# Kernel optimization log

Hardware: AMD Instinct MI355X
Metric: run time of the kernel (lower is better)

Reference implementation:

```python
import jax, jax.numpy as jnp
import numpy as np

B, T, F = 4096, 512, 8
U1, U2, DH = 8, 16, 16  # GRU1 units, GRU2 units, dense hidden


def _gru(x, W, Uw, b, units):
    """Keras GRU (v2, reset_after=True), activation=relu, recurrent_activation=sigmoid.
    x: [B, T, F_in]; W: [F_in, 3u]; Uw: [u, 3u]; b: [2, 3u]. Returns [B, T, u]."""
    bi, br = b[0], b[1]
    # precompute input projections for all timesteps: [T, B, 3u] (time-major for scan)
    gx = jnp.einsum('btf,fg->tbg', x, W) + bi
    u = units

    def step(h, xt):
        inner = h @ Uw + br                      # [B, 3u]
        z = jax.nn.sigmoid(xt[:, :u] + inner[:, :u])
        r = jax.nn.sigmoid(xt[:, u:2 * u] + inner[:, u:2 * u])
        hh = jax.nn.relu(xt[:, 2 * u:] + r * inner[:, 2 * u:])
        h = z * h + (1.0 - z) * hh
        return h, h

    h0 = jnp.zeros((x.shape[0], u), dtype=x.dtype)
    _, ys = jax.lax.scan(step, h0, gx)           # ys: [T, B, u]
    return jnp.transpose(ys, (1, 0, 2))          # [B, T, u]


def setup_inputs() -> dict:
    key = jax.random.key(0)
    ks = jax.random.split(key, 12)
    s = lambda fan_in: 1.0 / np.sqrt(fan_in)
    x = jax.random.normal(ks[0], (B, T, F), dtype=jnp.float32)
    W1 = jax.random.normal(ks[1], (F, 3 * U1), dtype=jnp.float32) * s(F)
    Ur1 = jax.random.normal(ks[2], (U1, 3 * U1), dtype=jnp.float32) * s(U1)
    b1 = jnp.zeros((2, 3 * U1), dtype=jnp.float32)
    W2 = jax.random.normal(ks[3], (U1, 3 * U2), dtype=jnp.float32) * s(U1)
    Ur2 = jax.random.normal(ks[4], (U2, 3 * U2), dtype=jnp.float32) * s(U2)
    b2 = jnp.zeros((2, 3 * U2), dtype=jnp.float32)
    Wd = jax.random.normal(ks[5], (U2, DH), dtype=jnp.float32) * 0.05  # random_normal init
    bd = jnp.zeros((DH,), dtype=jnp.float32)
    Wo = jax.random.normal(ks[6], (DH, 1), dtype=jnp.float32) * s(DH)
    bo = jnp.zeros((1,), dtype=jnp.float32)
    return {"x": x, "W1": W1, "Ur1": Ur1, "b1": b1, "W2": W2, "Ur2": Ur2,
            "b2": b2, "Wd": Wd, "bd": bd, "Wo": Wo, "bo": bo}


def reference(x, W1, Ur1, b1, W2, Ur2, b2, Wd, bd, Wo, bo):
    # Dropout layers are identity at inference (training=False)
    h = _gru(x, W1, Ur1, b1, U1)                 # [B, T, 8]
    h = _gru(h, W2, Ur2, b2, U2)                 # [B, T, 16]
    h = jax.nn.relu(h @ Wd + bd)                 # [B, T, 16]
    out = h @ Wo + bo                            # [B, T, 1]
    return out
```

## Files before the change

### kernel.cpp

```cpp
#include <hip/hip_runtime.h>

#define TT 512
#define LOG2E 1.44269504088896340736f

typedef float f2 __attribute__((ext_vector_type(2)));

template <int N>
__device__ __forceinline__ int rorki_(int v) {
    return __builtin_amdgcn_update_dpp(v, v, 0x120 + N, 0xf, 0xf, true);
}
template <int N>
__device__ __forceinline__ float rorkf_(float v) { return __int_as_float(rorki_<N>(__float_as_int(v))); }
template <int C>
__device__ __forceinline__ float shrf_(float v) {
    return __int_as_float(__builtin_amdgcn_update_dpp(0, __float_as_int(v), C, 0xf, 0xf, true));
}
__device__ __forceinline__ float sgm_(float v) {
    return __builtin_amdgcn_rcpf(1.f + __builtin_amdgcn_exp2f(-v));
}
__device__ __forceinline__ f2 pfma_(f2 a, f2 b, f2 c) {
    return __builtin_elementwise_fma(a, b, c);
}

__launch_bounds__(64)
__attribute__((amdgpu_waves_per_eu(1, 1)))
__global__ void gru_pk4(const float* __restrict__ x,
                        const float* __restrict__ W1, const float* __restrict__ Ur1,
                        const float* __restrict__ b1,
                        const float* __restrict__ W2, const float* __restrict__ Ur2,
                        const float* __restrict__ b2,
                        const float* __restrict__ Wd, const float* __restrict__ bd,
                        const float* __restrict__ Wo, const float* __restrict__ bo,
                        float* __restrict__ out)
{
    const int lane = threadIdx.x & 63;
    const int g    = lane >> 4;
    const int j    = lane & 15;
    const int u1   = j & 7;
    const int hi   = j >> 3;
    const int gcol = u1 + 8 * hi;
    const int row  = blockIdx.x * 4 + g;
    const bool ishi = (hi != 0);
    const bool isw  = (j == 15);

    const float* xbase = x + (size_t)blockIdx.x * 4 * TT * 8;
    const int    xoff  = g * TT * 8 + u1;
    float* outrow = out + (size_t)row * TT;

    int Lk[16];
    Lk[0]  = j;
    Lk[1]  = rorki_<1>(j);   Lk[2]  = rorki_<2>(j);   Lk[3]  = rorki_<3>(j);
    Lk[4]  = rorki_<4>(j);   Lk[5]  = rorki_<5>(j);   Lk[6]  = rorki_<6>(j);
    Lk[7]  = rorki_<7>(j);   Lk[8]  = rorki_<8>(j);   Lk[9]  = rorki_<9>(j);
    Lk[10] = rorki_<10>(j);  Lk[11] = rorki_<11>(j);  Lk[12] = rorki_<12>(j);
    Lk[13] = rorki_<13>(j);  Lk[14] = rorki_<14>(j);  Lk[15] = rorki_<15>(j);

    f2 Pz[8], Pr[8], Ph[8], Pd[8];
#pragma unroll
    for (int k = 0; k < 8; ++k) {
        const int a = Lk[2 * k], b = Lk[2 * k + 1];
        Pz[k] = f2{LOG2E * Ur2[a * 48 + j],      LOG2E * Ur2[b * 48 + j]};
        Pr[k] = f2{LOG2E * Ur2[a * 48 + 16 + j], LOG2E * Ur2[b * 48 + 16 + j]};
        Ph[k] = f2{Ur2[a * 48 + 32 + j],         Ur2[b * 48 + 32 + j]};
        Pd[k] = f2{Wd[a * 16 + j],               Wd[b * 16 + j]};
    }
    f2 Vz[4], Vr[4], Vh[4], VC[4], VQ[4];
    f2 Gx[4], Hx[4];
#pragma unroll
    for (int k = 0; k < 4; ++k) {
        const int a = Lk[2 * k] & 7, b = Lk[2 * k + 1] & 7;
        Vz[k] = f2{LOG2E * W2[a * 48 + j],       LOG2E * W2[b * 48 + j]};
        Vr[k] = f2{LOG2E * W2[a * 48 + 16 + j],  LOG2E * W2[b * 48 + 16 + j]};
        Vh[k] = f2{W2[a * 48 + 32 + j],          W2[b * 48 + 32 + j]};
        VC[k] = f2{LOG2E * Ur1[a * 24 + gcol],   LOG2E * Ur1[b * 24 + gcol]};
        VQ[k] = f2{Ur1[a * 24 + 16 + u1],        Ur1[b * 24 + 16 + u1]};
        Gx[k] = f2{LOG2E * W1[a * 24 + gcol],    LOG2E * W1[b * 24 + gcol]};
        Hx[k] = f2{W1[a * 24 + 16 + u1],         W1[b * 24 + 16 + u1]};
    }
    const float bAzr = LOG2E * (b1[gcol] + b1[24 + gcol]);
    const float bGh  = b1[16 + u1];
    const float bIh  = b1[40 + u1];
    const float bA2  = LOG2E * (b2[j] + b2[48 + j]);
    const float bB2  = LOG2E * (b2[16 + j] + b2[64 + j]);
    const float bC2  = b2[80 + j];
    const float bD2  = b2[32 + j];
    const float bdj  = bd[j], woj = Wo[j], boo = bo[0];

    float h1own = 0.f, h2own = 0.f;
    float azrP = bAzr, ihP = bIh;

    float xA = xbase[0 * 8 + xoff];
    float xB = xbase[1 * 8 + xoff];
    float xC = xbase[2 * 8 + xoff];

#define GSTEP(SS, XCUR, XFILL)                                                   \
    {                                                                            \
        const int s = (SS);                                                      \
                       \
        const float h0 = h2own;                                                  \
        f2 tp[8];                                                                \
        tp[0] = f2{h0,             rorkf_<1>(h0)};                               \
        tp[1] = f2{rorkf_<2>(h0),  rorkf_<3>(h0)};                               \
        tp[2] = f2{rorkf_<4>(h0),  rorkf_<5>(h0)};                               \
        tp[3] = f2{rorkf_<6>(h0),  rorkf_<7>(h0)};                               \
        tp[4] = f2{rorkf_<8>(h0),  rorkf_<9>(h0)};                               \
        tp[5] = f2{rorkf_<10>(h0), rorkf_<11>(h0)};                              \
        tp[6] = f2{rorkf_<12>(h0), rorkf_<13>(h0)};                              \
        tp[7] = f2{rorkf_<14>(h0), rorkf_<15>(h0)};                              \
        f2 za = f2{bA2, 0.f}, ra = f2{bB2, 0.f};                                 \
        f2 ha = f2{bC2, 0.f}, da = f2{bdj, 0.f};                                 \
        _Pragma("unroll")                                                        \
        for (int k = 0; k < 8; ++k) {                                            \
            za = pfma_(tp[k], Pz[k], za);  ra = pfma_(tp[k], Pr[k], ra);         \
            ha = pfma_(tp[k], Ph[k], ha);  da = pfma_(tp[k], Pd[k], da);         \
        }                                                                        \
                                     \
        const float x0 = XCUR;                                                   \
        f2 xp[4];                                                                \
        xp[0] = f2{x0,            rorkf_<1>(x0)};                                \
        xp[1] = f2{rorkf_<2>(x0), rorkf_<3>(x0)};                                \
        xp[2] = f2{rorkf_<4>(x0), rorkf_<5>(x0)};                                \
        xp[3] = f2{rorkf_<6>(x0), rorkf_<7>(x0)};                                \
        f2 axp = f2{azrP, 0.f}, ghp = f2{bGh, 0.f};                              \
        _Pragma("unroll")                                                        \
        for (int k = 0; k < 4; ++k) {                                            \
            axp = pfma_(xp[k], Gx[k], axp);  ghp = pfma_(xp[k], Hx[k], ghp);     \
        }                                                                        \
        XFILL = xbase[((s + 3) & (TT - 1)) * 8 + xoff];        \
                \
        const float azrC = axp.x + axp.y;                                        \
        const float s_own = sgm_(azrC);                                          \
        const float s_sw  = rorkf_<8>(s_own);                                    \
        const float z1 = ishi ? s_sw : s_own;                                    \
        const float r1 = ishi ? s_own : s_sw;                                    \
        const float ghxC = ghp.x + ghp.y;                                        \
        const float hh1 = fmaxf(fmaf(r1, ihP, ghxC), 0.f);                       \
        h1own = fmaf(z1, h1own - hh1, hh1);                                      \
                   \
        const float n0 = h1own;                                                  \
        f2 np[4];                                                                \
        np[0] = f2{n0,            rorkf_<1>(n0)};                                \
        np[1] = f2{rorkf_<2>(n0), rorkf_<3>(n0)};                                \
        np[2] = f2{rorkf_<4>(n0), rorkf_<5>(n0)};                                \
        np[3] = f2{rorkf_<6>(n0), rorkf_<7>(n0)};                                \
        f2 hbp = f2{bD2, 0.f}, aNp = f2{bAzr, 0.f}, iNp = f2{bIh, 0.f};          \
        _Pragma("unroll")                                                        \
        for (int k = 0; k < 4; ++k) {                                            \
            za  = pfma_(np[k], Vz[k], za);   ra  = pfma_(np[k], Vr[k], ra);      \
            hbp = pfma_(np[k], Vh[k], hbp);                                      \
            aNp = pfma_(np[k], VC[k], aNp);  iNp = pfma_(np[k], VQ[k], iNp);     \
        }                                                                        \
        azrP = aNp.x + aNp.y;  ihP = iNp.x + iNp.y;                              \
                                                  \
        const float zaC = za.x + za.y, raC = ra.x + ra.y;                        \
        const float haC = ha.x + ha.y, hbC = hbp.x + hbp.y;                      \
        const float z2 = sgm_(zaC), r2 = sgm_(raC);                              \
        const float hh2 = fmaxf(fmaf(r2, haC, hbC), 0.f);                        \
        h2own = fmaf(z2, h2own - hh2, hh2);                                      \
                                       \
        float e = fmaxf(da.x + da.y, 0.f) * woj;                                 \
        e += shrf_<0x118>(e);                                                    \
        e += shrf_<0x114>(e);                                                    \
        e += shrf_<0x112>(e);                                                    \
        e += shrf_<0x111>(e);                                                    \
        if (s > 0) { if (isw) outrow[s - 1] = e + boo; }                         \
    }

    for (int s0 = 0; s0 < TT; s0 += 4) {
        GSTEP(s0 + 0, xA, xA)
        GSTEP(s0 + 1, xB, xB)
        GSTEP(s0 + 2, xC, xC)
        GSTEP(s0 + 3, xA, xA)
        { float t = xB; xB = xC; xC = xA; xA = t; }
    }
#undef GSTEP

    {
        const float h0 = h2own;
        f2 tp[8];
        tp[0] = f2{h0,             rorkf_<1>(h0)};
        tp[1] = f2{rorkf_<2>(h0),  rorkf_<3>(h0)};
        tp[2] = f2{rorkf_<4>(h0),  rorkf_<5>(h0)};
        tp[3] = f2{rorkf_<6>(h0),  rorkf_<7>(h0)};
        tp[4] = f2{rorkf_<8>(h0),  rorkf_<9>(h0)};
        tp[5] = f2{rorkf_<10>(h0), rorkf_<11>(h0)};
        tp[6] = f2{rorkf_<12>(h0), rorkf_<13>(h0)};
        tp[7] = f2{rorkf_<14>(h0), rorkf_<15>(h0)};
        f2 da = f2{bdj, 0.f};
#pragma unroll
        for (int k = 0; k < 8; ++k) da = pfma_(tp[k], Pd[k], da);
        float e = fmaxf(da.x + da.y, 0.f) * woj;
        e += shrf_<0x118>(e);
        e += shrf_<0x114>(e);
        e += shrf_<0x112>(e);
        e += shrf_<0x111>(e);
        if (isw) outrow[TT - 1] = e + boo;
    }
}

extern "C" void kernel_launch(void* const* d_in, const int* in_sizes, int n_in,
                              void* d_out, int out_size, void* d_ws, size_t ws_size,
                              hipStream_t stream) {
    const float* x   = (const float*)d_in[0];
    const float* W1  = (const float*)d_in[1];
    const float* Ur1 = (const float*)d_in[2];
    const float* b1  = (const float*)d_in[3];
    const float* W2  = (const float*)d_in[4];
    const float* Ur2 = (const float*)d_in[5];
    const float* b2  = (const float*)d_in[6];
    const float* Wd  = (const float*)d_in[7];
    const float* bd  = (const float*)d_in[8];
    const float* Wo  = (const float*)d_in[9];
    const float* bo  = (const float*)d_in[10];
    float* out = (float*)d_out;

    dim3 grid(4096 / 4);
    dim3 block(64);
    gru_pk4<<<grid, block, 0, stream>>>(x, W1, Ur1, b1, W2, Ur2, b2,
                                        Wd, bd, Wo, bo, out);
}
```

Baseline: 174.6 us.

## Split GRU layers across two wavefronts with chunked LDS pipeline

```diff
diff --git a/kernel.cpp b/kernel.cpp
--- a/kernel.cpp
+++ b/kernel.cpp
@@ -1,6 +1,9 @@
 #include <hip/hip_runtime.h>
 
 #define TT 512
+#define CH 32
+#define NCH 16
+#define NPH (NCH + 2)
 #define LOG2E 1.44269504088896340736f
 
 typedef float f2 __attribute__((ext_vector_type(2)));
@@ -22,30 +25,30 @@
     return __builtin_elementwise_fma(a, b, c);
 }
 
-__launch_bounds__(64)
-__attribute__((amdgpu_waves_per_eu(1, 1)))
-__global__ void gru_pk4(const float* __restrict__ x,
-                        const float* __restrict__ W1, const float* __restrict__ Ur1,
-                        const float* __restrict__ b1,
-                        const float* __restrict__ W2, const float* __restrict__ Ur2,
-                        const float* __restrict__ b2,
-                        const float* __restrict__ Wd, const float* __restrict__ bd,
-                        const float* __restrict__ Wo, const float* __restrict__ bo,
-                        float* __restrict__ out)
+__launch_bounds__(128)
+__attribute__((amdgpu_waves_per_eu(2, 2)))
+__global__ void gru_ws(const float* __restrict__ x,
+                       const float* __restrict__ W1, const float* __restrict__ Ur1,
+                       const float* __restrict__ b1,
+                       const float* __restrict__ W2, const float* __restrict__ Ur2,
+                       const float* __restrict__ b2,
+                       const float* __restrict__ Wd, const float* __restrict__ bd,
+                       const float* __restrict__ Wo, const float* __restrict__ bo,
+                       float* __restrict__ out)
 {
-    const int lane = threadIdx.x & 63;
+    __shared__ float h1b[2][CH][4][8];
+    __shared__ float h2b[2][CH][4][16];
+
+    const int tid  = threadIdx.x;
+    const int wv   = tid >> 6;
+    const int lane = tid & 63;
     const int g    = lane >> 4;
     const int j    = lane & 15;
     const int u1   = j & 7;
     const int hi   = j >> 3;
     const int gcol = u1 + 8 * hi;
-    const int row  = blockIdx.x * 4 + g;
     const bool ishi = (hi != 0);
     const bool isw  = (j == 15);
-
-    const float* xbase = x + (size_t)blockIdx.x * 4 * TT * 8;
-    const int    xoff  = g * TT * 8 + u1;
-    float* outrow = out + (size_t)row * TT;
 
     int Lk[16];
     Lk[0]  = j;
@@ -55,146 +58,208 @@
     Lk[10] = rorki_<10>(j);  Lk[11] = rorki_<11>(j);  Lk[12] = rorki_<12>(j);
     Lk[13] = rorki_<13>(j);  Lk[14] = rorki_<14>(j);  Lk[15] = rorki_<15>(j);
 
-    f2 Pz[8], Pr[8], Ph[8], Pd[8];
-#pragma unroll
-    for (int k = 0; k < 8; ++k) {
-        const int a = Lk[2 * k], b = Lk[2 * k + 1];
-        Pz[k] = f2{LOG2E * Ur2[a * 48 + j],      LOG2E * Ur2[b * 48 + j]};
-        Pr[k] = f2{LOG2E * Ur2[a * 48 + 16 + j], LOG2E * Ur2[b * 48 + 16 + j]};
-        Ph[k] = f2{Ur2[a * 48 + 32 + j],         Ur2[b * 48 + 32 + j]};
-        Pd[k] = f2{Wd[a * 16 + j],               Wd[b * 16 + j]};
-    }
-    f2 Vz[4], Vr[4], Vh[4], VC[4], VQ[4];
-    f2 Gx[4], Hx[4];
-#pragma unroll
-    for (int k = 0; k < 4; ++k) {
-        const int a = Lk[2 * k] & 7, b = Lk[2 * k + 1] & 7;
-        Vz[k] = f2{LOG2E * W2[a * 48 + j],       LOG2E * W2[b * 48 + j]};
-        Vr[k] = f2{LOG2E * W2[a * 48 + 16 + j],  LOG2E * W2[b * 48 + 16 + j]};
-        Vh[k] = f2{W2[a * 48 + 32 + j],          W2[b * 48 + 32 + j]};
-        VC[k] = f2{LOG2E * Ur1[a * 24 + gcol],   LOG2E * Ur1[b * 24 + gcol]};
-        VQ[k] = f2{Ur1[a * 24 + 16 + u1],        Ur1[b * 24 + 16 + u1]};
-        Gx[k] = f2{LOG2E * W1[a * 24 + gcol],    LOG2E * W1[b * 24 + gcol]};
-        Hx[k] = f2{W1[a * 24 + 16 + u1],         W1[b * 24 + 16 + u1]};
-    }
-    const float bAzr = LOG2E * (b1[gcol] + b1[24 + gcol]);
-    const float bGh  = b1[16 + u1];
-    const float bIh  = b1[40 + u1];
-    const float bA2  = LOG2E * (b2[j] + b2[48 + j]);
-    const float bB2  = LOG2E * (b2[16 + j] + b2[64 + j]);
-    const float bC2  = b2[80 + j];
-    const float bD2  = b2[32 + j];
-    const float bdj  = bd[j], woj = Wo[j], boo = bo[0];
-
-    float h1own = 0.f, h2own = 0.f;
-    float azrP = bAzr, ihP = bIh;
-
-    float xA = xbase[0 * 8 + xoff];
-    float xB = xbase[1 * 8 + xoff];
-    float xC = xbase[2 * 8 + xoff];
-
-#define GSTEP(SS, XCUR, XFILL)                                                   \
-    {                                                                            \
-        const int s = (SS);                                                      \
-                       \
-        const float h0 = h2own;                                                  \
-        f2 tp[8];                                                                \
-        tp[0] = f2{h0,             rorkf_<1>(h0)};                               \
-        tp[1] = f2{rorkf_<2>(h0),  rorkf_<3>(h0)};                               \
-        tp[2] = f2{rorkf_<4>(h0),  rorkf_<5>(h0)};                               \
-        tp[3] = f2{rorkf_<6>(h0),  rorkf_<7>(h0)};                               \
-        tp[4] = f2{rorkf_<8>(h0),  rorkf_<9>(h0)};                               \
-        tp[5] = f2{rorkf_<10>(h0), rorkf_<11>(h0)};                              \
-        tp[6] = f2{rorkf_<12>(h0), rorkf_<13>(h0)};                              \
-        tp[7] = f2{rorkf_<14>(h0), rorkf_<15>(h0)};                              \
-        f2 za = f2{bA2, 0.f}, ra = f2{bB2, 0.f};                                 \
-        f2 ha = f2{bC2, 0.f}, da = f2{bdj, 0.f};                                 \
-        _Pragma("unroll")                                                        \
-        for (int k = 0; k < 8; ++k) {                                            \
-            za = pfma_(tp[k], Pz[k], za);  ra = pfma_(tp[k], Pr[k], ra);         \
-            ha = pfma_(tp[k], Ph[k], ha);  da = pfma_(tp[k], Pd[k], da);         \
-        }                                                                        \
-                                     \
-        const float x0 = XCUR;                                                   \
-        f2 xp[4];                                                                \
-        xp[0] = f2{x0,            rorkf_<1>(x0)};                                \
-        xp[1] = f2{rorkf_<2>(x0), rorkf_<3>(x0)};                                \
-        xp[2] = f2{rorkf_<4>(x0), rorkf_<5>(x0)};                                \
-        xp[3] = f2{rorkf_<6>(x0), rorkf_<7>(x0)};                                \
-        f2 axp = f2{azrP, 0.f}, ghp = f2{bGh, 0.f};                              \
-        _Pragma("unroll")                                                        \
-        for (int k = 0; k < 4; ++k) {                                            \
-            axp = pfma_(xp[k], Gx[k], axp);  ghp = pfma_(xp[k], Hx[k], ghp);     \
-        }                                                                        \
-        XFILL = xbase[((s + 3) & (TT - 1)) * 8 + xoff];        \
-                \
-        const float azrC = axp.x + axp.y;                                        \
-        const float s_own = sgm_(azrC);                                          \
-        const float s_sw  = rorkf_<8>(s_own);                                    \
-        const float z1 = ishi ? s_sw : s_own;                                    \
-        const float r1 = ishi ? s_own : s_sw;                                    \
-        const float ghxC = ghp.x + ghp.y;                                        \
-        const float hh1 = fmaxf(fmaf(r1, ihP, ghxC), 0.f);                       \
-        h1own = fmaf(z1, h1own - hh1, hh1);                                      \
-                   \
-        const float n0 = h1own;                                                  \
-        f2 np[4];                                                                \
-        np[0] = f2{n0,            rorkf_<1>(n0)};                                \
-        np[1] = f2{rorkf_<2>(n0), rorkf_<3>(n0)};                                \
-        np[2] = f2{rorkf_<4>(n0), rorkf_<5>(n0)};                                \
-        np[3] = f2{rorkf_<6>(n0), rorkf_<7>(n0)};                                \
-        f2 hbp = f2{bD2, 0.f}, aNp = f2{bAzr, 0.f}, iNp = f2{bIh, 0.f};          \
-        _Pragma("unroll")                                                        \
-        for (int k = 0; k < 4; ++k) {                                            \
-            za  = pfma_(np[k], Vz[k], za);   ra  = pfma_(np[k], Vr[k], ra);      \
-            hbp = pfma_(np[k], Vh[k], hbp);                                      \
-            aNp = pfma_(np[k], VC[k], aNp);  iNp = pfma_(np[k], VQ[k], iNp);     \
-        }                                                                        \
-        azrP = aNp.x + aNp.y;  ihP = iNp.x + iNp.y;                              \
-                                                  \
-        const float zaC = za.x + za.y, raC = ra.x + ra.y;                        \
-        const float haC = ha.x + ha.y, hbC = hbp.x + hbp.y;                      \
-        const float z2 = sgm_(zaC), r2 = sgm_(raC);                              \
-        const float hh2 = fmaxf(fmaf(r2, haC, hbC), 0.f);                        \
-        h2own = fmaf(z2, h2own - hh2, hh2);                                      \
-                                       \
-        float e = fmaxf(da.x + da.y, 0.f) * woj;                                 \
-        e += shrf_<0x118>(e);                                                    \
-        e += shrf_<0x114>(e);                                                    \
-        e += shrf_<0x112>(e);                                                    \
-        e += shrf_<0x111>(e);                                                    \
-        if (s > 0) { if (isw) outrow[s - 1] = e + boo; }                         \
-    }
-
-    for (int s0 = 0; s0 < TT; s0 += 4) {
-        GSTEP(s0 + 0, xA, xA)
-        GSTEP(s0 + 1, xB, xB)
-        GSTEP(s0 + 2, xC, xC)
-        GSTEP(s0 + 3, xA, xA)
-        { float t = xB; xB = xC; xC = xA; xA = t; }
-    }
-#undef GSTEP
-
-    {
-        const float h0 = h2own;
-        f2 tp[8];
-        tp[0] = f2{h0,             rorkf_<1>(h0)};
-        tp[1] = f2{rorkf_<2>(h0),  rorkf_<3>(h0)};
-        tp[2] = f2{rorkf_<4>(h0),  rorkf_<5>(h0)};
-        tp[3] = f2{rorkf_<6>(h0),  rorkf_<7>(h0)};
-        tp[4] = f2{rorkf_<8>(h0),  rorkf_<9>(h0)};
-        tp[5] = f2{rorkf_<10>(h0), rorkf_<11>(h0)};
-        tp[6] = f2{rorkf_<12>(h0), rorkf_<13>(h0)};
-        tp[7] = f2{rorkf_<14>(h0), rorkf_<15>(h0)};
-        f2 da = f2{bdj, 0.f};
-#pragma unroll
-        for (int k = 0; k < 8; ++k) da = pfma_(tp[k], Pd[k], da);
-        float e = fmaxf(da.x + da.y, 0.f) * woj;
-        e += shrf_<0x118>(e);
-        e += shrf_<0x114>(e);
-        e += shrf_<0x112>(e);
-        e += shrf_<0x111>(e);
-        if (isw) outrow[TT - 1] = e + boo;
+    if (wv == 0) {
+        f2 Gx[4], Hx[4], VC[4], VQ[4];
+#pragma unroll
+        for (int k = 0; k < 4; ++k) {
+            const int a = Lk[2 * k] & 7, b = Lk[2 * k + 1] & 7;
+            Gx[k] = f2{LOG2E * W1[a * 24 + gcol],  LOG2E * W1[b * 24 + gcol]};
+            Hx[k] = f2{W1[a * 24 + 16 + u1],       W1[b * 24 + 16 + u1]};
+            VC[k] = f2{LOG2E * Ur1[a * 24 + gcol], LOG2E * Ur1[b * 24 + gcol]};
+            VQ[k] = f2{Ur1[a * 24 + 16 + u1],      Ur1[b * 24 + 16 + u1]};
+        }
+        f2 Pd[8];
+#pragma unroll
+        for (int k = 0; k < 8; ++k)
+            Pd[k] = f2{Wd[(2 * k) * 16 + j], Wd[(2 * k + 1) * 16 + j]};
+        const float bAzr = LOG2E * (b1[gcol] + b1[24 + gcol]);
+        const float bGh  = b1[16 + u1];
+        const float bIh  = b1[40 + u1];
+        const float bdj  = bd[j], woj = Wo[j], boo = bo[0];
+
+        const float* xbase = x + (size_t)blockIdx.x * 4 * TT * 8;
+        const int    xoff  = g * TT * 8 + u1;
+        float* outrow = out + (size_t)(blockIdx.x * 4 + g) * TT;
+
+        float h1own = 0.f, azrP = bAzr, ihP = bIh;
+        float xA = xbase[0 * 8 + xoff];
+        float xB = xbase[1 * 8 + xoff];
+        float xC = xbase[2 * 8 + xoff];
+        float4 hA0, hA1, hA2, hA3, hB0, hB1, hB2, hB3;
+
+#define G1STEP(TG, SL, XCUR, XFILL)                                          \
+    {                                                                        \
+        const float x0 = XCUR;                                               \
+        const f2 xp0 = f2{x0,            rorkf_<1>(x0)};                     \
+        const f2 xp1 = f2{rorkf_<2>(x0), rorkf_<3>(x0)};                     \
+        const f2 xp2 = f2{rorkf_<4>(x0), rorkf_<5>(x0)};                     \
+        const f2 xp3 = f2{rorkf_<6>(x0), rorkf_<7>(x0)};                     \
+        f2 axp = f2{azrP, 0.f}, ghp = f2{bGh, 0.f};                          \
+        axp = pfma_(xp0, Gx[0], axp);  ghp = pfma_(xp0, Hx[0], ghp);         \
+        axp = pfma_(xp1, Gx[1], axp);  ghp = pfma_(xp1, Hx[1], ghp);         \
+        axp = pfma_(xp2, Gx[2], axp);  ghp = pfma_(xp2, Hx[2], ghp);         \
+        axp = pfma_(xp3, Gx[3], axp);  ghp = pfma_(xp3, Hx[3], ghp);         \
+        XFILL = xbase[(((TG) + 3) & (TT - 1)) * 8 + xoff];                   \
+        const float azrC = axp.x + axp.y;                                    \
+        const float s_own = sgm_(azrC);                                      \
+        const float s_sw  = rorkf_<8>(s_own);                                \
+        const float z1 = ishi ? s_sw : s_own;                                \
+        const float r1 = ishi ? s_own : s_sw;                                \
+        const float hh1 = fmaxf(fmaf(r1, ihP, ghp.x + ghp.y), 0.f);          \
+        h1own = fmaf(z1, h1own - hh1, hh1);                                  \
+        const float n0 = h1own;                                              \
+        const f2 np0 = f2{n0,            rorkf_<1>(n0)};                     \
+        const f2 np1 = f2{rorkf_<2>(n0), rorkf_<3>(n0)};                     \
+        const f2 np2 = f2{rorkf_<4>(n0), rorkf_<5>(n0)};                     \
+        const f2 np3 = f2{rorkf_<6>(n0), rorkf_<7>(n0)};                     \
+        f2 aNp = f2{bAzr, 0.f}, iNp = f2{bIh, 0.f};                          \
+        aNp = pfma_(np0, VC[0], aNp);  iNp = pfma_(np0, VQ[0], iNp);         \
+        aNp = pfma_(np1, VC[1], aNp);  iNp = pfma_(np1, VQ[1], iNp);         \
+        aNp = pfma_(np2, VC[2], aNp);  iNp = pfma_(np2, VQ[2], iNp);         \
+        aNp = pfma_(np3, VC[3], aNp);  iNp = pfma_(np3, VQ[3], iNp);         \
+        azrP = aNp.x + aNp.y;  ihP = iNp.x + iNp.y;                          \
+        h1b[p & 1][SL][g][u1] = h1own;                                       \
+    }
+
+#define DSTEP(DL, C0, C1, C2, C3, N0, N1, N2, N3, DN)                        \
+    {                                                                        \
+        f2 da = f2{bdj, 0.f};                                                \
+        da = pfma_(f2{C0.x, C0.y}, Pd[0], da);                               \
+        da = pfma_(f2{C0.z, C0.w}, Pd[1], da);                               \
+        da = pfma_(f2{C1.x, C1.y}, Pd[2], da);                               \
+        da = pfma_(f2{C1.z, C1.w}, Pd[3], da);                               \
+        da = pfma_(f2{C2.x, C2.y}, Pd[4], da);                               \
+        da = pfma_(f2{C2.z, C2.w}, Pd[5], da);                               \
+        da = pfma_(f2{C3.x, C3.y}, Pd[6], da);                               \
+        da = pfma_(f2{C3.z, C3.w}, Pd[7], da);                               \
+        N0 = *(const float4*)&h2b[p & 1][DN][g][0];                          \
+        N1 = *(const float4*)&h2b[p & 1][DN][g][4];                          \
+        N2 = *(const float4*)&h2b[p & 1][DN][g][8];                          \
+        N3 = *(const float4*)&h2b[p & 1][DN][g][12];                         \
+        float e = fmaxf(da.x + da.y, 0.f) * woj;                             \
+        e += shrf_<0x118>(e);                                                \
+        e += shrf_<0x114>(e);                                                \
+        e += shrf_<0x112>(e);                                                \
+        e += shrf_<0x111>(e);                                                \
+        if (isw) outd[DL] = e + boo;                                         \
+    }
+
+        for (int p = 0; p < NPH; ++p) {
+            if (p < 2) {
+                const int t0 = p * CH;
+                for (int s = 0; s < CH; s += 4) {
+                    G1STEP(t0 + s + 0, s + 0, xA, xA)
+                    G1STEP(t0 + s + 1, s + 1, xB, xB)
+                    G1STEP(t0 + s + 2, s + 2, xC, xC)
+                    G1STEP(t0 + s + 3, s + 3, xA, xA)
+                    { float t = xB; xB = xC; xC = xA; xA = t; }
+                }
+            } else if (p < NCH) {
+                const int t0 = p * CH;
+                float* outd = outrow + (p - 2) * CH;
+                hA0 = *(const float4*)&h2b[p & 1][0][g][0];
+                hA1 = *(const float4*)&h2b[p & 1][0][g][4];
+                hA2 = *(const float4*)&h2b[p & 1][0][g][8];
+                hA3 = *(const float4*)&h2b[p & 1][0][g][12];
+                for (int s = 0; s < CH; s += 4) {
+                    G1STEP(t0 + s + 0, s + 0, xA, xA)
+                    DSTEP(s + 0, hA0, hA1, hA2, hA3, hB0, hB1, hB2, hB3, s + 1)
+                    G1STEP(t0 + s + 1, s + 1, xB, xB)
+                    DSTEP(s + 1, hB0, hB1, hB2, hB3, hA0, hA1, hA2, hA3, s + 2)
+                    G1STEP(t0 + s + 2, s + 2, xC, xC)
+                    DSTEP(s + 2, hA0, hA1, hA2, hA3, hB0, hB1, hB2, hB3, s + 3)
+                    G1STEP(t0 + s + 3, s + 3, xA, xA)
+                    DSTEP(s + 3, hB0, hB1, hB2, hB3, hA0, hA1, hA2, hA3, (s + 4) & (CH - 1))
+                    { float t = xB; xB = xC; xC = xA; xA = t; }
+                }
+            } else {
+                float* outd = outrow + (p - 2) * CH;
+                hA0 = *(const float4*)&h2b[p & 1][0][g][0];
+                hA1 = *(const float4*)&h2b[p & 1][0][g][4];
+                hA2 = *(const float4*)&h2b[p & 1][0][g][8];
+                hA3 = *(const float4*)&h2b[p & 1][0][g][12];
+                for (int s = 0; s < CH; s += 4) {
+                    DSTEP(s + 0, hA0, hA1, hA2, hA3, hB0, hB1, hB2, hB3, s + 1)
+                    DSTEP(s + 1, hB0, hB1, hB2, hB3, hA0, hA1, hA2, hA3, s + 2)
+                    DSTEP(s + 2, hA0, hA1, hA2, hA3, hB0, hB1, hB2, hB3, s + 3)
+                    DSTEP(s + 3, hB0, hB1, hB2, hB3, hA0, hA1, hA2, hA3, (s + 4) & (CH - 1))
+                }
+            }
+            __syncthreads();
+        }
+#undef G1STEP
+#undef DSTEP
+    } else {
+        f2 Pz[8], Pr[8], Ph[8];
+#pragma unroll
+        for (int k = 0; k < 8; ++k) {
+            const int a = Lk[2 * k], b = Lk[2 * k + 1];
+            Pz[k] = f2{LOG2E * Ur2[a * 48 + j],      LOG2E * Ur2[b * 48 + j]};
+            Pr[k] = f2{LOG2E * Ur2[a * 48 + 16 + j], LOG2E * Ur2[b * 48 + 16 + j]};
+            Ph[k] = f2{Ur2[a * 48 + 32 + j],         Ur2[b * 48 + 32 + j]};
+        }
+        f2 Vz[4], Vr[4], Vh[4];
+#pragma unroll
+        for (int k = 0; k < 4; ++k) {
+            Vz[k] = f2{LOG2E * W2[(2 * k) * 48 + j],      LOG2E * W2[(2 * k + 1) * 48 + j]};
+            Vr[k] = f2{LOG2E * W2[(2 * k) * 48 + 16 + j], LOG2E * W2[(2 * k + 1) * 48 + 16 + j]};
+            Vh[k] = f2{W2[(2 * k) * 48 + 32 + j],         W2[(2 * k + 1) * 48 + 32 + j]};
+        }
+        const float bA2 = LOG2E * (b2[j] + b2[48 + j]);
+        const float bB2 = LOG2E * (b2[16 + j] + b2[64 + j]);
+        const float bC2 = b2[80 + j];
+        const float bD2 = b2[32 + j];
+
+        float h2own = 0.f;
+        float4 kA0, kA1, kB0, kB1;
+
+#define G2STEP(SL, K0, K1, M0, M1, SN)                                       \
+    {                                                                        \
+        const float h0 = h2own;                                              \
+        const f2 tp0 = f2{h0,             rorkf_<1>(h0)};                    \
+        const f2 tp1 = f2{rorkf_<2>(h0),  rorkf_<3>(h0)};                    \
+        const f2 tp2 = f2{rorkf_<4>(h0),  rorkf_<5>(h0)};                    \
+        const f2 tp3 = f2{rorkf_<6>(h0),  rorkf_<7>(h0)};                    \
+        const f2 tp4 = f2{rorkf_<8>(h0),  rorkf_<9>(h0)};                    \
+        const f2 tp5 = f2{rorkf_<10>(h0), rorkf_<11>(h0)};                   \
+        const f2 tp6 = f2{rorkf_<12>(h0), rorkf_<13>(h0)};                   \
+        const f2 tp7 = f2{rorkf_<14>(h0), rorkf_<15>(h0)};                   \
+        f2 za = f2{bA2, 0.f}, ra = f2{bB2, 0.f}, ha = f2{bC2, 0.f};          \
+        za = pfma_(tp0, Pz[0], za); ra = pfma_(tp0, Pr[0], ra); ha = pfma_(tp0, Ph[0], ha); \
+        za = pfma_(tp1, Pz[1], za); ra = pfma_(tp1, Pr[1], ra); ha = pfma_(tp1, Ph[1], ha); \
+        za = pfma_(tp2, Pz[2], za); ra = pfma_(tp2, Pr[2], ra); ha = pfma_(tp2, Ph[2], ha); \
+        za = pfma_(tp3, Pz[3], za); ra = pfma_(tp3, Pr[3], ra); ha = pfma_(tp3, Ph[3], ha); \
+        za = pfma_(tp4, Pz[4], za); ra = pfma_(tp4, Pr[4], ra); ha = pfma_(tp4, Ph[4], ha); \
+        za = pfma_(tp5, Pz[5], za); ra = pfma_(tp5, Pr[5], ra); ha = pfma_(tp5, Ph[5], ha); \
+        za = pfma_(tp6, Pz[6], za); ra = pfma_(tp6, Pr[6], ra); ha = pfma_(tp6, Ph[6], ha); \
+        za = pfma_(tp7, Pz[7], za); ra = pfma_(tp7, Pr[7], ra); ha = pfma_(tp7, Ph[7], ha); \
+        const f2 q0 = f2{K0.x, K0.y}, q1 = f2{K0.z, K0.w};                   \
+        const f2 q2 = f2{K1.x, K1.y}, q3 = f2{K1.z, K1.w};                   \
+        f2 hbp = f2{bD2, 0.f};                                               \
+        za = pfma_(q0, Vz[0], za); ra = pfma_(q0, Vr[0], ra); hbp = pfma_(q0, Vh[0], hbp); \
+        za = pfma_(q1, Vz[1], za); ra = pfma_(q1, Vr[1], ra); hbp = pfma_(q1, Vh[1], hbp); \
+        za = pfma_(q2, Vz[2], za); ra = pfma_(q2, Vr[2], ra); hbp = pfma_(q2, Vh[2], hbp); \
+        za = pfma_(q3, Vz[3], za); ra = pfma_(q3, Vr[3], ra); hbp = pfma_(q3, Vh[3], hbp); \
+        M0 = *(const float4*)&h1b[(p - 1) & 1][SN][g][0];                    \
+        M1 = *(const float4*)&h1b[(p - 1) & 1][SN][g][4];                    \
+        const float z2 = sgm_(za.x + za.y), r2 = sgm_(ra.x + ra.y);          \
+        const float hh2 = fmaxf(fmaf(r2, ha.x + ha.y, hbp.x + hbp.y), 0.f);  \
+        h2own = fmaf(z2, h2own - hh2, hh2);                                  \
+        h2b[(p - 1) & 1][SL][g][j] = h2own;                                  \
+    }
+
+        for (int p = 0; p < NPH; ++p) {
+            if (p >= 1 && p <= NCH) {
+                kA0 = *(const float4*)&h1b[(p - 1) & 1][0][g][0];
+                kA1 = *(const float4*)&h1b[(p - 1) & 1][0][g][4];
+                for (int s = 0; s < CH; s += 2) {
+                    G2STEP(s + 0, kA0, kA1, kB0, kB1, s + 1)
+                    G2STEP(s + 1, kB0, kB1, kA0, kA1, (s + 2) & (CH - 1))
+                }
+            }
+            __syncthreads();
+        }
+#undef G2STEP
     }
 }
 
@@ -215,7 +280,7 @@
     float* out = (float*)d_out;
 
     dim3 grid(4096 / 4);
-    dim3 block(64);
-    gru_pk4<<<grid, block, 0, stream>>>(x, W1, Ur1, b1, W2, Ur2, b2,
-                                        Wd, bd, Wo, bo, out);
-}
+    dim3 block(128);
+    gru_ws<<<grid, block, 0, stream>>>(x, W1, Ur1, b1, W2, Ur2, b2,
+                                       Wd, bd, Wo, bo, out);
+}
```

Result: faster. 164.8 us (-5.6%).
